# Optimization experiments

Hardware: AMD Instinct MI355X
Metric: run time of the kernel (lower is better)

Reference implementation:

```python
import jax, jax.numpy as jnp
import numpy as np

B, S, D, H = 4, 2048, 2048, 16
DK = D // H

def setup_inputs() -> dict:
    key = jax.random.key(0)
    ks = jax.random.split(key, 9)
    def xavier(k, shape):
        fan_in, fan_out = shape[1], shape[0]
        limit = (6.0 / (fan_in + fan_out)) ** 0.5
        return jax.random.uniform(k, shape, jnp.float32, -limit, limit)
    return {
        "x": jax.random.normal(ks[0], (B, S, D), jnp.float32),
        "Wq": xavier(ks[1], (D, D)), "bq": jnp.zeros((D,), jnp.float32),
        "Wk": xavier(ks[2], (D, D)), "bk": jnp.zeros((D,), jnp.float32),
        "Wv": xavier(ks[3], (D, D)), "bv": jnp.zeros((D,), jnp.float32),
        "Wo": xavier(ks[4], (D, D)), "bo": jnp.zeros((D,), jnp.float32),
    }

def reference(x, Wq, bq, Wk, bk, Wv, bv, Wo, bo):
    b, s, d = x.shape
    scale = DK ** 0.5
    # torch nn.Linear: y = x @ W.T + b
    def proj(W, bias):
        y = jnp.einsum('bsd,ed->bse', x, W) + bias
        return y.reshape(b, s, H, DK).transpose(0, 2, 1, 3)  # (b, h, s, dk)
    Q, K, V = proj(Wq, bq), proj(Wk, bk), proj(Wv, bv)
    scores = jnp.einsum('bhqd,bhkd->bhqk', Q, K) / scale
    causal = jnp.triu(jnp.ones((s, s), dtype=bool), k=1)
    scores = jnp.where(causal[None, None], -jnp.inf, scores)
    attn = jax.nn.softmax(scores, axis=-1)
    ctx = jnp.einsum('bhqk,bhkd->bhqd', attn, V)
    ctx = ctx.transpose(0, 2, 1, 3).reshape(b, s, d)
    out = jnp.einsum('bsd,ed->bse', ctx, Wo) + bo
    return out
```

## Files before the change

### kernel.cpp

```cpp
#include <hip/hip_runtime.h>
#include <hip/hip_bf16.h>
#include <cstdint>

#define B_  4
#define S_  2048
#define D_  2048
#define H_  16
#define DK_ 128

typedef __attribute__((ext_vector_type(8))) short short8;
typedef __attribute__((ext_vector_type(4))) short s16x4;
typedef __attribute__((ext_vector_type(4))) float f32x4;
typedef unsigned short ushort_t;

__device__ __forceinline__ void gl_lds16(const void* g, void* l) {
  __builtin_amdgcn_global_load_lds(
      (const __attribute__((address_space(1))) uint32_t*)g,
      (__attribute__((address_space(3))) uint32_t*)l, 16, 0, 0);
}

__device__ __forceinline__ ushort_t f2bf(float f) {
  __hip_bfloat16 h = __float2bfloat16(f);
  return *(ushort_t*)&h;
}

__global__ __launch_bounds__(256) void cvt_all(
    const float* __restrict__ x,  const float* __restrict__ w0,
    const float* __restrict__ w1, const float* __restrict__ w2,
    const float* __restrict__ w3, ushort_t* __restrict__ dst)
{
  constexpr size_t NE = (size_t)B_ * S_ * D_;
  constexpr size_t NW = (size_t)D_ * D_;
  constexpr int XB = (int)(NE / 8 / 256);
  constexpr int WB = (int)(NW / 8 / 256);

  const int blk = blockIdx.x;
  const float* src;
  size_t base;
  int li;
  if (blk < XB)           { src = x;  base = 0;           li = blk * 256 + threadIdx.x; }
  else if (blk < XB+WB)   { src = w0; base = NE/8;        li = (blk-XB)     * 256 + threadIdx.x; }
  else if (blk < XB+2*WB) { src = w1; base = (NE+NW)/8;   li = (blk-XB-WB)  * 256 + threadIdx.x; }
  else if (blk < XB+3*WB) { src = w2; base = (NE+2*NW)/8; li = (blk-XB-2*WB)* 256 + threadIdx.x; }
  else                    { src = w3; base = (NE+3*NW)/8; li = (blk-XB-3*WB)* 256 + threadIdx.x; }

  float4 a = ((const float4*)src)[li * 2];
  float4 b = ((const float4*)src)[li * 2 + 1];
  short8 o;
  o[0] = (short)f2bf(a.x); o[1] = (short)f2bf(a.y);
  o[2] = (short)f2bf(a.z); o[3] = (short)f2bf(a.w);
  o[4] = (short)f2bf(b.x); o[5] = (short)f2bf(b.y);
  o[6] = (short)f2bf(b.z); o[7] = (short)f2bf(b.w);
  ((short8*)dst)[base + li] = o;
}

#define STAGE_A(q, tt) do {                                                \
    int r0_ = (q) * 64 + w * 8;                                            \
    gl_lds16(Agb + (size_t)(r0_ + lr) * 2048 + (tt) * 64 + lc, &As[r0_ * 64]); \
    r0_ += 128;                                                            \
    gl_lds16(Agb + (size_t)(r0_ + lr) * 2048 + (tt) * 64 + lc, &As[r0_ * 64]); \
  } while (0)
#define STAGE_B(q, tt) do {                                                \
    int r0_ = (w >> 1) * 64 + (q) * 32 + ((w & 1) * 2) * 8;                \
    gl_lds16(Wgb + (size_t)(r0_ + lr) * 2048 + (tt) * 64 + lc, &Bs[r0_ * 64]); \
    r0_ += 8;                                                              \
    gl_lds16(Wgb + (size_t)(r0_ + lr) * 2048 + (tt) * 64 + lc, &Bs[r0_ * 64]); \
  } while (0)

#define GEMM_BODY()                                                               \
  f32x4 acc[8][4] = {};                                                           \
  short8 aA[4][2];                                                                \
  short8 bB[2][2][2];                                                             \
  STAGE_A(0, 0); STAGE_A(1, 0); STAGE_B(0, 0); STAGE_B(1, 0);                     \
  asm volatile("s_waitcnt vmcnt(0)" ::: "memory");                                \
  __builtin_amdgcn_s_barrier();                                                   \
  for (int kt = 0; kt < NT; ++kt) {                                               \
                     \
    _Pragma("unroll")                                                             \
    for (int fm = 0; fm < 4; ++fm)                                                \
      _Pragma("unroll")                                                           \
      for (int kk = 0; kk < 2; ++kk) {                                            \
        const int row = wm * 128 + fm * 16 + l15;                                 \
        aA[fm][kk] = *(const short8*)&As[row * 64 + (((kk * 4 + lhi) ^ (l15 & 7)) << 3)]; \
      }                                                                           \
    _Pragma("unroll")                                                             \
    for (int fn = 0; fn < 2; ++fn)                                                \
      _Pragma("unroll")                                                           \
      for (int kk = 0; kk < 2; ++kk) {                                            \
        const int row = wn * 64 + fn * 16 + l15;                                  \
        bB[0][fn][kk] = *(const short8*)&Bs[row * 64 + (((kk * 4 + lhi) ^ (l15 & 7)) << 3)]; \
      }                                                                           \
    __builtin_amdgcn_s_barrier();                                                 \
    __builtin_amdgcn_s_setprio(1);                                                \
    _Pragma("unroll")                                                             \
    for (int kk = 0; kk < 2; ++kk)                                                \
      _Pragma("unroll")                                                           \
      for (int fm = 0; fm < 4; ++fm)                                              \
        _Pragma("unroll")                                                         \
        for (int fn = 0; fn < 2; ++fn)                                            \
          acc[fm][fn] = __builtin_amdgcn_mfma_f32_16x16x32_bf16(aA[fm][kk], bB[0][fn][kk], acc[fm][fn], 0, 0, 0); \
    __builtin_amdgcn_s_setprio(0);                                                \
    asm volatile("s_waitcnt vmcnt(2)" ::: "memory");           \
    __builtin_amdgcn_s_barrier();                                                 \
         \
    _Pragma("unroll")                                                             \
    for (int fn = 0; fn < 2; ++fn)                                                \
      _Pragma("unroll")                                                           \
      for (int kk = 0; kk < 2; ++kk) {                                            \
        const int row = wn * 64 + 32 + fn * 16 + l15;                             \
        bB[1][fn][kk] = *(const short8*)&Bs[row * 64 + (((kk * 4 + lhi) ^ (l15 & 7)) << 3)]; \
      }                                                                           \
    if (kt + 1 < NT) { STAGE_A(0, kt + 1); STAGE_B(0, kt + 1); }                  \
    __builtin_amdgcn_s_barrier();                                                 \
    __builtin_amdgcn_s_setprio(1);                                                \
    _Pragma("unroll")                                                             \
    for (int kk = 0; kk < 2; ++kk)                                                \
      _Pragma("unroll")                                                           \
      for (int fm = 0; fm < 4; ++fm)                                              \
        _Pragma("unroll")                                                         \
        for (int fn = 0; fn < 2; ++fn)                                            \
          acc[fm][2 + fn] = __builtin_amdgcn_mfma_f32_16x16x32_bf16(aA[fm][kk], bB[1][fn][kk], acc[fm][2 + fn], 0, 0, 0); \
    __builtin_amdgcn_s_setprio(0);                                                \
    if (kt + 1 < NT) { asm volatile("s_waitcnt vmcnt(4)" ::: "memory"); }         \
    else             { asm volatile("s_waitcnt vmcnt(0)" ::: "memory"); }         \
    __builtin_amdgcn_s_barrier();                         \
                   \
    _Pragma("unroll")                                                             \
    for (int fm = 0; fm < 4; ++fm)                                                \
      _Pragma("unroll")                                                           \
      for (int kk = 0; kk < 2; ++kk) {                                            \
        const int row = wm * 128 + 64 + fm * 16 + l15;                            \
        aA[fm][kk] = *(const short8*)&As[row * 64 + (((kk * 4 + lhi) ^ (l15 & 7)) << 3)]; \
      }                                                                           \
    if (kt + 1 < NT) STAGE_B(1, kt + 1);                                          \
    __builtin_amdgcn_s_barrier();                                                 \
    __builtin_amdgcn_s_setprio(1);                                                \
    _Pragma("unroll")                                                             \
    for (int kk = 0; kk < 2; ++kk)                                                \
      _Pragma("unroll")                                                           \
      for (int fm = 0; fm < 4; ++fm)                                              \
        _Pragma("unroll")                                                         \
        for (int fn = 0; fn < 2; ++fn)                                            \
          acc[4 + fm][fn] = __builtin_amdgcn_mfma_f32_16x16x32_bf16(aA[fm][kk], bB[0][fn][kk], acc[4 + fm][fn], 0, 0, 0); \
    __builtin_amdgcn_s_setprio(0);                                                \
    __builtin_amdgcn_s_barrier();                                                 \
                               \
    if (kt + 1 < NT) STAGE_A(1, kt + 1);                                          \
    __builtin_amdgcn_s_setprio(1);                                                \
    _Pragma("unroll")                                                             \
    for (int kk = 0; kk < 2; ++kk)                                                \
      _Pragma("unroll")                                                           \
      for (int fm = 0; fm < 4; ++fm)                                              \
        _Pragma("unroll")                                                         \
        for (int fn = 0; fn < 2; ++fn)                                            \
          acc[4 + fm][2 + fn] = __builtin_amdgcn_mfma_f32_16x16x32_bf16(aA[fm][kk], bB[1][fn][kk], acc[4 + fm][2 + fn], 0, 0, 0); \
    __builtin_amdgcn_s_setprio(0);                                                \
    if (kt + 1 < NT) { asm volatile("s_waitcnt vmcnt(4)" ::: "memory"); }         \
    else             { asm volatile("s_waitcnt vmcnt(0)" ::: "memory"); }         \
    __builtin_amdgcn_s_barrier();                     \
  }

__global__ __launch_bounds__(512, 2) void gemmQKV(
    const ushort_t* __restrict__ A,
    const ushort_t* __restrict__ Wqm, const ushort_t* __restrict__ Wkm,
    const ushort_t* __restrict__ Wvm,
    const float* __restrict__ bq, const float* __restrict__ bk,
    const float* __restrict__ bv,
    ushort_t* __restrict__ Qo, ushort_t* __restrict__ Ko,
    ushort_t* __restrict__ Vo)
{
  constexpr int NT = D_ / 64;

  __shared__ ushort_t As[256 * 64];
  __shared__ ushort_t Bs[256 * 64];

  const int bid = blockIdx.x;
  const int c = bid & 7;
  const int j0 = bid >> 3;
  const int proj = j0 >> 5;
  const int s = j0 & 31;
  const int tnl = s & 7;
  const int tm = c * 4 + (s >> 3);

  const ushort_t* Wsel = (proj == 0) ? Wqm : (proj == 1) ? Wkm : Wvm;
  const float*    bsel = (proj == 0) ? bq  : (proj == 1) ? bk  : bv;
  ushort_t*       osel = (proj == 0) ? Qo  : (proj == 1) ? Ko  : Vo;

  const int t = threadIdx.x;
  const int l = t & 63;
  const int w = t >> 6;
  const int wm = w >> 2;
  const int wn = w & 3;
  const int l15 = l & 15, lhi = l >> 4;
  const int lr = l >> 3;
  const int lc = ((l & 7) ^ lr) * 8;

  const ushort_t* Agb = A + (size_t)(tm * 256) * 2048;
  const ushort_t* Wgb = Wsel + (size_t)(tnl * 256) * 2048;

  GEMM_BODY()

  if (proj == 2) {
#pragma unroll
    for (int qn = 0; qn < 2; ++qn)
#pragma unroll
      for (int fn = 0; fn < 2; ++fn) {
        const int e = tnl * 256 + wn * 64 + qn * 32 + fn * 16 + l15;
        const float bvv = bsel[e];
        const int h = e >> 7, dk = e & (DK_ - 1);
#pragma unroll
        for (int qm = 0; qm < 2; ++qm)
#pragma unroll
          for (int fm = 0; fm < 4; ++fm) {
            const int srow0 = tm * 256 + wm * 128 + qm * 64 + fm * 16 + lhi * 4;
            const f32x4 v4 = acc[qm * 4 + fm][qn * 2 + fn];
            const int b = srow0 >> 11, s0 = srow0 & (S_ - 1);
            s16x4 pk;
#pragma unroll
            for (int r = 0; r < 4; ++r) pk[r] = (short)f2bf(v4[r] + bvv);
            *(s16x4*)(osel + (((size_t)b * H_ + h) * DK_ + dk) * S_ + s0) = pk;
          }
      }
  } else {
#pragma unroll
    for (int qm = 0; qm < 2; ++qm)
#pragma unroll
      for (int qn = 0; qn < 2; ++qn) {
        __syncthreads();
#pragma unroll
        for (int fn = 0; fn < 2; ++fn) {
          const int e = tnl * 256 + wn * 64 + qn * 32 + fn * 16 + l15;
          const float bvv = bsel[e];
          const int lcol = wn * 32 + fn * 16 + l15;
#pragma unroll
          for (int fm = 0; fm < 4; ++fm) {
            const f32x4 v4 = acc[qm * 4 + fm][qn * 2 + fn];
#pragma unroll
            for (int r = 0; r < 4; ++r) {
              const int lrow = wm * 64 + fm * 16 + lhi * 4 + r;
              As[lrow * 128 + (lcol ^ ((lrow & 7) << 3))] = f2bf(v4[r] + bvv);
            }
          }
        }
        __syncthreads();
        {
          const int erow = t >> 2;
          const int eli  = t & 3;
          const int grow = tm * 256 + (erow >> 6) * 128 + qm * 64 + (erow & 63);
          const int bb = grow >> 11, sR = grow & (S_ - 1);
#pragma unroll
          for (int wnb = 0; wnb < 4; ++wnb) {
            const int lcol = wnb * 32 + eli * 8;
            short8 v = *(const short8*)&As[erow * 128 + (lcol ^ ((erow & 7) << 3))];
            const int col = wnb * 64 + qn * 32 + eli * 8;
            const int e2 = tnl * 256 + col;
            const int h = e2 >> 7, dk = e2 & (DK_ - 1);
            *(short8*)(osel + (((size_t)bb * H_ + h) * S_ + sR) * DK_ + dk) = v;
          }
        }
      }
  }
}

__global__ __launch_bounds__(512, 2) void gemmOut(
    const ushort_t* __restrict__ A,
    const ushort_t* __restrict__ W,
    const float* __restrict__ bias,
    float* __restrict__ outp)
{
  constexpr int NT = D_ / 64;
  constexpr int NWG = (B_ * S_ / 256) * (D_ / 256);

  __shared__ ushort_t As[256 * 64];
  __shared__ ushort_t Bs[256 * 64];

  const int bid = blockIdx.x;
  const int swz = (bid & 7) * (NWG / 8) + (bid >> 3);
  const int tm = swz >> 3;
  const int tn = swz & 7;

  const int t = threadIdx.x;
  const int l = t & 63;
  const int w = t >> 6;
  const int wm = w >> 2;
  const int wn = w & 3;
  const int l15 = l & 15, lhi = l >> 4;
  const int lr = l >> 3;
  const int lc = ((l & 7) ^ lr) * 8;

  const ushort_t* Agb = A + (size_t)(tm * 256) * 2048;
  const ushort_t* Wgb = W + (size_t)(tn * 256) * 2048;

  GEMM_BODY()

#pragma unroll
  for (int qn = 0; qn < 2; ++qn)
#pragma unroll
    for (int fn = 0; fn < 2; ++fn) {
      const int e = tn * 256 + wn * 64 + qn * 32 + fn * 16 + l15;
      const float bvv = bias[e];
#pragma unroll
      for (int qm = 0; qm < 2; ++qm)
#pragma unroll
        for (int fm = 0; fm < 4; ++fm) {
          const int srow0 = tm * 256 + wm * 128 + qm * 64 + fm * 16 + lhi * 4;
          const f32x4 v4 = acc[qm * 4 + fm][qn * 2 + fn];
#pragma unroll
          for (int r = 0; r < 4; ++r)
            outp[(size_t)(srow0 + r) * D_ + e] = v4[r] + bvv;
        }
    }
}
#undef STAGE_A
#undef STAGE_B
#undef GEMM_BODY

__global__ __launch_bounds__(256, 2) void attn_kern(
    const ushort_t* __restrict__ Q,
    const ushort_t* __restrict__ K,
    const ushort_t* __restrict__ Vt,
    ushort_t* __restrict__ C)
{
  __shared__ ushort_t Ks[2][64 * 128];
  __shared__ ushort_t Vs[2][128 * 64];
  __shared__ ushort_t Pl[4][32 * 64];

  const int bid = blockIdx.x;
  const int i = bid >> 3;
  const int bh = (bid & 7) * 8 + (i >> 3);
  const int qp = i & 7;

  const ushort_t* Qg = Q + (size_t)bh * S_ * DK_;
  const ushort_t* Kg = K + (size_t)bh * S_ * DK_;
  const ushort_t* Vg = Vt + (size_t)bh * DK_ * S_;
  const int b = bh >> 4, h = bh & 15;

  const int t = threadIdx.x;
  const int l = t & 63;
  const int w = t >> 6;
  const int l15 = l & 15, lhi = l >> 4;

  const float cs = 0.08838834764831845f * 1.4426950408889634f;
  const float DEFER_RAW = 8.0f / cs;

  short8 ones;
#pragma unroll
  for (int j = 0; j < 8; ++j) ones[j] = (short)0x3F80;

  int koff[4], voff[4];
#pragma unroll
  for (int j = 0; j < 4; ++j) {
    const int krow = w * 16 + j * 4 + lhi;
    koff[j] = krow * DK_ + 8 * (l15 ^ ((j * 4 + lhi) & 7));
    const int vrow = (w * 4 + j) * 8 + (l >> 3);
    voff[j] = vrow * S_ + 8 * ((l & 7) ^ (l >> 3));
  }
  int kcol[4];
#pragma unroll
  for (int kt = 0; kt < 4; ++kt)
    kcol[kt] = ((kt * 64 + lhi * 16) ^ ((l15 & 7) << 4)) >> 1;
  int vcol[2];
#pragma unroll
  for (int hb = 0; hb < 2; ++hb)
    vcol[hb] = ((hb * 64 + lhi * 16) ^ ((l15 & 7) << 4)) >> 1;

#define STAGE_KV(pb, kvv) do {                                              \
    _Pragma("unroll")                                                       \
    for (int j = 0; j < 4; ++j) {                                           \
      gl_lds16(Kg + (size_t)(kvv) * DK_ + koff[j], Ks[pb] + (w * 4 + j) * 512); \
      gl_lds16(Vg + (size_t)(kvv) + voff[j],       Vs[pb] + (w * 4 + j) * 512); \
    }                                                                       \
  } while (0)

  for (int pass = 0; pass < 2; ++pass) {
    const int qb = pass ? (15 - qp) : qp;
    const int qrow0 = qb * 128 + w * 32;
    const int nkv = 2 * (qb + 1);

    short8 qa[2][4];
#pragma unroll
    for (int rf = 0; rf < 2; ++rf)
#pragma unroll
      for (int kt = 0; kt < 4; ++kt)
        qa[rf][kt] = *(const short8*)(Qg + (size_t)(qrow0 + rf * 16 + l15) * DK_ + kt * 32 + lhi * 8);

    f32x4 o[2][8] = {};
    f32x4 lsum[2] = {};
    float mrow[2][4];
#pragma unroll
    for (int rf = 0; rf < 2; ++rf)
#pragma unroll
      for (int r = 0; r < 4; ++r) mrow[rf][r] = -1e30f;

    STAGE_KV(0, 0);
    asm volatile("s_waitcnt vmcnt(0)" ::: "memory");
    __syncthreads();

    for (int kvt = 0; kvt < nkv; ++kvt) {
      const int kv = kvt * 64;
      const int p = kvt & 1;

      if (kvt + 1 < nkv) STAGE_KV(p ^ 1, kv + 64);

      f32x4 sf[2][4] = {};
      __builtin_amdgcn_s_setprio(1);
#pragma unroll
      for (int f = 0; f < 4; ++f) {
#pragma unroll
        for (int kt = 0; kt < 4; ++kt) {
          short8 kb = *(const short8*)(Ks[p] + (f * 16 + l15) * 128 + kcol[kt]);
          sf[0][f] = __builtin_amdgcn_mfma_f32_16x16x32_bf16(qa[0][kt], kb, sf[0][f], 0, 0, 0);
          sf[1][f] = __builtin_amdgcn_mfma_f32_16x16x32_bf16(qa[1][kt], kb, sf[1][f], 0, 0, 0);
        }
      }
      __builtin_amdgcn_s_setprio(0);

      float pmax[2][4];
#pragma unroll
      for (int rf = 0; rf < 2; ++rf)
#pragma unroll
        for (int r = 0; r < 4; ++r) pmax[rf][r] = -1e30f;
      const bool domask = (kv + 63 > qrow0);
      if (domask) {
#pragma unroll
        for (int f = 0; f < 4; ++f) {
          const int col = kv + f * 16 + l15;
#pragma unroll
          for (int rf = 0; rf < 2; ++rf)
#pragma unroll
            for (int r = 0; r < 4; ++r) {
              const int row = qrow0 + rf * 16 + lhi * 4 + r;
              if (col > row) sf[rf][f][r] = -1e30f;
              pmax[rf][r] = fmaxf(pmax[rf][r], sf[rf][f][r]);
            }
        }
      } else {
#pragma unroll
        for (int f = 0; f < 4; ++f)
#pragma unroll
          for (int rf = 0; rf < 2; ++rf)
#pragma unroll
            for (int r = 0; r < 4; ++r)
              pmax[rf][r] = fmaxf(pmax[rf][r], sf[rf][f][r]);
      }
#pragma unroll
      for (int d = 1; d < 16; d <<= 1)
#pragma unroll
        for (int rf = 0; rf < 2; ++rf)
#pragma unroll
          for (int r = 0; r < 4; ++r)
            pmax[rf][r] = fmaxf(pmax[rf][r], __shfl_xor(pmax[rf][r], d, 64));

      bool need = false;
#pragma unroll
      for (int rf = 0; rf < 2; ++rf)
#pragma unroll
        for (int r = 0; r < 4; ++r) need |= (pmax[rf][r] > mrow[rf][r] + DEFER_RAW);
      if (__any(need)) {
#pragma unroll
        for (int rf = 0; rf < 2; ++rf)
#pragma unroll
          for (int r = 0; r < 4; ++r) {
            const float mn = fmaxf(mrow[rf][r], pmax[rf][r]);
            const float alpha = __builtin_amdgcn_exp2f((mrow[rf][r] - mn) * cs);
            mrow[rf][r] = mn;
            lsum[rf][r] *= alpha;
#pragma unroll
            for (int n = 0; n < 8; ++n) o[rf][n][r] *= alpha;
          }
      }

      ushort_t* P = Pl[w];
#pragma unroll
      for (int f = 0; f < 4; ++f)
#pragma unroll
        for (int rf = 0; rf < 2; ++rf)
#pragma unroll
          for (int r = 0; r < 4; ++r) {
            const float pv = __builtin_amdgcn_exp2f((sf[rf][f][r] - mrow[rf][r]) * cs);
            const int prow = rf * 16 + lhi * 4 + r;
            P[prow * 64 + ((f * 16 + l15) ^ ((prow & 7) << 3))] = f2bf(pv);
          }

      asm volatile("s_waitcnt lgkmcnt(0)" ::: "memory");
      short8 pa[2][2];
#pragma unroll
      for (int rf = 0; rf < 2; ++rf)
#pragma unroll
        for (int ks = 0; ks < 2; ++ks) {
          const int prow = rf * 16 + l15;
          pa[rf][ks] = *(const short8*)(P + prow * 64 + ((ks * 32 + lhi * 8) ^ ((prow & 7) << 3)));
        }

      __builtin_amdgcn_s_setprio(1);
#pragma unroll
      for (int rf = 0; rf < 2; ++rf) {
        lsum[rf] = __builtin_amdgcn_mfma_f32_16x16x32_bf16(pa[rf][0], ones, lsum[rf], 0, 0, 0);
        lsum[rf] = __builtin_amdgcn_mfma_f32_16x16x32_bf16(pa[rf][1], ones, lsum[rf], 0, 0, 0);
      }
#pragma unroll
      for (int n = 0; n < 8; ++n) {
#pragma unroll
        for (int hb = 0; hb < 2; ++hb) {
          short8 vb = *(const short8*)(Vs[p] + (n * 16 + l15) * 64 + vcol[hb]);
          o[0][n] = __builtin_amdgcn_mfma_f32_16x16x32_bf16(pa[0][hb], vb, o[0][n], 0, 0, 0);
          o[1][n] = __builtin_amdgcn_mfma_f32_16x16x32_bf16(pa[1][hb], vb, o[1][n], 0, 0, 0);
        }
      }
      __builtin_amdgcn_s_setprio(0);

      asm volatile("s_waitcnt vmcnt(0)" ::: "memory");
      __syncthreads();
    }

#pragma unroll
    for (int rf = 0; rf < 2; ++rf) {
      float linv[4];
#pragma unroll
      for (int r = 0; r < 4; ++r) linv[r] = 1.0f / lsum[rf][r];
#pragma unroll
      for (int n = 0; n < 8; ++n) {
        const int dk = n * 16 + l15;
#pragma unroll
        for (int r = 0; r < 4; ++r) {
          const int srow = qrow0 + rf * 16 + lhi * 4 + r;
          C[(((size_t)b * S_ + srow) * H_ + h) * DK_ + dk] = f2bf(o[rf][n][r] * linv[r]);
        }
      }
    }
  }
#undef STAGE_KV
}

extern "C" void kernel_launch(void* const* d_in, const int* in_sizes, int n_in,
                              void* d_out, int out_size, void* d_ws, size_t ws_size,
                              hipStream_t stream) {
  const float* x  = (const float*)d_in[0];
  const float* Wq = (const float*)d_in[1];
  const float* bq = (const float*)d_in[2];
  const float* Wk = (const float*)d_in[3];
  const float* bk = (const float*)d_in[4];
  const float* Wv = (const float*)d_in[5];
  const float* bv = (const float*)d_in[6];
  const float* Wo = (const float*)d_in[7];
  const float* bo = (const float*)d_in[8];
  float* out = (float*)d_out;

  ushort_t* ws = (ushort_t*)d_ws;
  const size_t NE = (size_t)B_ * S_ * D_;
  const size_t NW = (size_t)D_ * D_;
  ushort_t* xb  = ws;
  ushort_t* Wqb = ws + NE;
  ushort_t* Wkb = Wqb + NW;
  ushort_t* Wvb = Wkb + NW;
  ushort_t* Wob = Wvb + NW;
  ushort_t* Qw  = Wob + NW;
  ushort_t* Kw  = Qw + NE;
  ushort_t* Vw  = Kw + NE;
  ushort_t* Cw  = xb;

  const int XB = (int)(NE / 8 / 256);
  const int WB = (int)(NW / 8 / 256);
  cvt_all<<<dim3(XB + 4 * WB), dim3(256), 0, stream>>>(x, Wq, Wk, Wv, Wo, ws);

  gemmQKV<<<dim3(768), dim3(512), 0, stream>>>(xb, Wqb, Wkb, Wvb, bq, bk, bv, Qw, Kw, Vw);
  attn_kern<<<dim3(512), dim3(256), 0, stream>>>(Qw, Kw, Vw, Cw);
  gemmOut<<<dim3(256), dim3(512), 0, stream>>>(Cw, Wob, bo, out);
}
```

Before: 402.4 us.

## Load GEMM weight fragments directly from global into registers, dropping LDS staging for B

Result: slower. 564.6 us (+40.3%).

```diff
diff --git a/kernel.cpp b/kernel.cpp
--- a/kernel.cpp
+++ b/kernel.cpp
@@ -60,35 +60,35 @@
     r0_ += 128;                                                            \
     gl_lds16(Agb + (size_t)(r0_ + lr) * 2048 + (tt) * 64 + lc, &As[r0_ * 64]); \
   } while (0)
-#define STAGE_B(q, tt) do {                                                \
-    int r0_ = (w >> 1) * 64 + (q) * 32 + ((w & 1) * 2) * 8;                \
-    gl_lds16(Wgb + (size_t)(r0_ + lr) * 2048 + (tt) * 64 + lc, &Bs[r0_ * 64]); \
-    r0_ += 8;                                                              \
-    gl_lds16(Wgb + (size_t)(r0_ + lr) * 2048 + (tt) * 64 + lc, &Bs[r0_ * 64]); \
+
+#define LDB_G(tt) do {                                                     \
+    _Pragma("unroll")                                                      \
+    for (int qn_ = 0; qn_ < 2; ++qn_)                                      \
+      _Pragma("unroll")                                                    \
+      for (int fn_ = 0; fn_ < 2; ++fn_)                                    \
+        _Pragma("unroll")                                                  \
+        for (int kk_ = 0; kk_ < 2; ++kk_)                                  \
+          bB[qn_][fn_][kk_] = *(const short8*)(Bgl + (size_t)(qn_ * 32 + fn_ * 16) * 2048 + (tt) * 64 + kk_ * 32); \
   } while (0)
 
 #define GEMM_BODY()                                                               \
   f32x4 acc[8][4] = {};                                                           \
   short8 aA[4][2];                                                                \
   short8 bB[2][2][2];                                                             \
-  STAGE_A(0, 0); STAGE_A(1, 0); STAGE_B(0, 0); STAGE_B(1, 0);                     \
-  asm volatile("s_waitcnt vmcnt(0)" ::: "memory");                                \
+  const ushort_t* Bgl = Wgb + (size_t)(wn * 64 + l15) * 2048 + lhi * 8;           \
+  LDB_G(0);                                                                       \
+  STAGE_A(0, 0); STAGE_A(1, 0);                                                   \
+  asm volatile("s_waitcnt vmcnt(2)" ::: "memory");          \
   __builtin_amdgcn_s_barrier();                                                   \
   for (int kt = 0; kt < NT; ++kt) {                                               \
-                     \
+    const bool stg = (kt + 1 < NT);                                               \
+                 \
     _Pragma("unroll")                                                             \
     for (int fm = 0; fm < 4; ++fm)                                                \
       _Pragma("unroll")                                                           \
       for (int kk = 0; kk < 2; ++kk) {                                            \
         const int row = wm * 128 + fm * 16 + l15;                                 \
         aA[fm][kk] = *(const short8*)&As[row * 64 + (((kk * 4 + lhi) ^ (l15 & 7)) << 3)]; \
-      }                                                                           \
-    _Pragma("unroll")                                                             \
-    for (int fn = 0; fn < 2; ++fn)                                                \
-      _Pragma("unroll")                                                           \
-      for (int kk = 0; kk < 2; ++kk) {                                            \
-        const int row = wn * 64 + fn * 16 + l15;                                  \
-        bB[0][fn][kk] = *(const short8*)&Bs[row * 64 + (((kk * 4 + lhi) ^ (l15 & 7)) << 3)]; \
       }                                                                           \
     __builtin_amdgcn_s_barrier();                                                 \
     __builtin_amdgcn_s_setprio(1);                                                \
@@ -100,17 +100,9 @@
         for (int fn = 0; fn < 2; ++fn)                                            \
           acc[fm][fn] = __builtin_amdgcn_mfma_f32_16x16x32_bf16(aA[fm][kk], bB[0][fn][kk], acc[fm][fn], 0, 0, 0); \
     __builtin_amdgcn_s_setprio(0);                                                \
-    asm volatile("s_waitcnt vmcnt(2)" ::: "memory");           \
-    __builtin_amdgcn_s_barrier();                                                 \
-         \
-    _Pragma("unroll")                                                             \
-    for (int fn = 0; fn < 2; ++fn)                                                \
-      _Pragma("unroll")                                                           \
-      for (int kk = 0; kk < 2; ++kk) {                                            \
-        const int row = wn * 64 + 32 + fn * 16 + l15;                             \
-        bB[1][fn][kk] = *(const short8*)&Bs[row * 64 + (((kk * 4 + lhi) ^ (l15 & 7)) << 3)]; \
-      }                                                                           \
-    if (kt + 1 < NT) { STAGE_A(0, kt + 1); STAGE_B(0, kt + 1); }                  \
+    __builtin_amdgcn_s_barrier();                                                 \
+                    \
+    if (stg) STAGE_A(0, kt + 1);                                                  \
     __builtin_amdgcn_s_barrier();                                                 \
     __builtin_amdgcn_s_setprio(1);                                                \
     _Pragma("unroll")                                                             \
@@ -121,10 +113,10 @@
         for (int fn = 0; fn < 2; ++fn)                                            \
           acc[fm][2 + fn] = __builtin_amdgcn_mfma_f32_16x16x32_bf16(aA[fm][kk], bB[1][fn][kk], acc[fm][2 + fn], 0, 0, 0); \
     __builtin_amdgcn_s_setprio(0);                                                \
-    if (kt + 1 < NT) { asm volatile("s_waitcnt vmcnt(4)" ::: "memory"); }         \
-    else             { asm volatile("s_waitcnt vmcnt(0)" ::: "memory"); }         \
-    __builtin_amdgcn_s_barrier();                         \
-                   \
+    if (stg) { asm volatile("s_waitcnt vmcnt(2)" ::: "memory"); }    \
+    else     { asm volatile("s_waitcnt vmcnt(0)" ::: "memory"); }                 \
+    __builtin_amdgcn_s_barrier();                                                 \
+                         \
     _Pragma("unroll")                                                             \
     for (int fm = 0; fm < 4; ++fm)                                                \
       _Pragma("unroll")                                                           \
@@ -132,7 +124,6 @@
         const int row = wm * 128 + 64 + fm * 16 + l15;                            \
         aA[fm][kk] = *(const short8*)&As[row * 64 + (((kk * 4 + lhi) ^ (l15 & 7)) << 3)]; \
       }                                                                           \
-    if (kt + 1 < NT) STAGE_B(1, kt + 1);                                          \
     __builtin_amdgcn_s_barrier();                                                 \
     __builtin_amdgcn_s_setprio(1);                                                \
     _Pragma("unroll")                                                             \
@@ -144,8 +135,8 @@
           acc[4 + fm][fn] = __builtin_amdgcn_mfma_f32_16x16x32_bf16(aA[fm][kk], bB[0][fn][kk], acc[4 + fm][fn], 0, 0, 0); \
     __builtin_amdgcn_s_setprio(0);                                                \
     __builtin_amdgcn_s_barrier();                                                 \
-                               \
-    if (kt + 1 < NT) STAGE_A(1, kt + 1);                                          \
+          \
+    if (stg) STAGE_A(1, kt + 1);                                                  \
     __builtin_amdgcn_s_setprio(1);                                                \
     _Pragma("unroll")                                                             \
     for (int kk = 0; kk < 2; ++kk)                                                \
@@ -155,9 +146,10 @@
         for (int fn = 0; fn < 2; ++fn)                                            \
           acc[4 + fm][2 + fn] = __builtin_amdgcn_mfma_f32_16x16x32_bf16(aA[fm][kk], bB[1][fn][kk], acc[4 + fm][2 + fn], 0, 0, 0); \
     __builtin_amdgcn_s_setprio(0);                                                \
-    if (kt + 1 < NT) { asm volatile("s_waitcnt vmcnt(4)" ::: "memory"); }         \
-    else             { asm volatile("s_waitcnt vmcnt(0)" ::: "memory"); }         \
-    __builtin_amdgcn_s_barrier();                     \
+    if (stg) LDB_G(kt + 1);                                                       \
+    if (stg) { asm volatile("s_waitcnt vmcnt(10)" ::: "memory"); } \
+    else     { asm volatile("s_waitcnt vmcnt(0)" ::: "memory"); }                 \
+    __builtin_amdgcn_s_barrier();                                                 \
   }
 
 __global__ __launch_bounds__(512, 2) void gemmQKV(
@@ -172,7 +164,6 @@
   constexpr int NT = D_ / 64;
 
   __shared__ ushort_t As[256 * 64];
-  __shared__ ushort_t Bs[256 * 64];
 
   const int bid = blockIdx.x;
   const int c = bid & 7;
@@ -272,7 +263,6 @@
   constexpr int NWG = (B_ * S_ / 256) * (D_ / 256);
 
   __shared__ ushort_t As[256 * 64];
-  __shared__ ushort_t Bs[256 * 64];
 
   const int bid = blockIdx.x;
   const int swz = (bid & 7) * (NWG / 8) + (bid >> 3);
@@ -312,7 +302,7 @@
     }
 }
 #undef STAGE_A
-#undef STAGE_B
+#undef LDB_G
 #undef GEMM_BODY
 
 __global__ __launch_bounds__(256, 2) void attn_kern(
```
